# Optimization experiments

Hardware: AMD Instinct MI355X
Metric: run time of the kernel (lower is better)

## Reference

```python
import jax, jax.numpy as jnp
import numpy as np

T = 2048          # tokens
HID = 4096        # hidden_size
H = 32            # n_heads
D = 192           # head_dim
DR = 64           # qk_rope_head_dim
Q_LORA = 1536
O_LORA = 512
G = 4             # o_groups
EPS = 1e-6
MAX_POS = 4096
ROPE_BASE = 10000.0
SCALE = D ** -0.5


def _rmsnorm(x, weight=None, eps=EPS):
    # normalize over last dim in fp32, like the triton kernel / RMSNorm
    xf = x.astype(jnp.float32)
    rms_inv = jax.lax.rsqrt(jnp.mean(xf * xf, axis=-1, keepdims=True) + eps)
    out = xf * rms_inv
    if weight is not None:
        out = out * weight
    return out.astype(x.dtype)


def _apply_rope(x, cos, sin):
    # x: [..., DR]; interleaved complex rotation (deepseek-style freqs_cis mult)
    x2 = x.reshape(x.shape[:-1] + (DR // 2, 2))
    a, b = x2[..., 0], x2[..., 1]
    ra = a * cos - b * sin
    rb = a * sin + b * cos
    return jnp.stack([ra, rb], axis=-1).reshape(x.shape)


def setup_inputs() -> dict:
    key = jax.random.key(0)
    ks = jax.random.split(key, 12)
    s = lambda k, shape, scale: jax.random.normal(k, shape, dtype=jnp.float32) * scale
    x = s(ks[0], (T, HID), 1.0)
    positions = jnp.arange(T, dtype=jnp.int64)
    wq_a = s(ks[1], (Q_LORA, HID), HID ** -0.5)
    q_norm_w = jnp.ones((Q_LORA,), jnp.float32)
    wq_b = s(ks[2], (H * D, Q_LORA), Q_LORA ** -0.5)
    wkv = s(ks[3], (D, HID), HID ** -0.5)
    kv_norm_w = jnp.ones((D,), jnp.float32)
    attn_sink = s(ks[4], (H,), 1.0)
    wo_a = s(ks[5], (G * O_LORA, (H * D) // G), ((H * D) // G) ** -0.5)
    wo_b = s(ks[6], (HID, G * O_LORA), (G * O_LORA) ** -0.5)
    # precomputed rope tables [MAX_POS, DR//2]
    inv_freq = 1.0 / (ROPE_BASE ** (np.arange(0, DR, 2, dtype=np.float32) / DR))
    t = np.arange(MAX_POS, dtype=np.float32)
    freqs = np.outer(t, inv_freq)
    rope_cos = jnp.asarray(np.cos(freqs))
    rope_sin = jnp.asarray(np.sin(freqs))
    return dict(x=x, positions=positions, wq_a=wq_a, q_norm_w=q_norm_w, wq_b=wq_b,
                wkv=wkv, kv_norm_w=kv_norm_w, attn_sink=attn_sink, wo_a=wo_a,
                wo_b=wo_b, rope_cos=rope_cos, rope_sin=rope_sin)


def reference(x, positions, wq_a, q_norm_w, wq_b, wkv, kv_norm_w, attn_sink,
              wo_a, wo_b, rope_cos, rope_sin):
    cos = rope_cos[positions]  # [T, DR//2]
    sin = rope_sin[positions]

    # q path: wq_a -> RMSNorm(weighted) -> wq_b -> per-head unweighted RMSNorm -> RoPE
    q_lora = _rmsnorm(x @ wq_a.T, q_norm_w)                # [T, Q_LORA]
    q = (q_lora @ wq_b.T).reshape(T, H, D)                 # [T, H, D]
    q = _rmsnorm(q)                                        # per-head rms_normalize
    q_rope = _apply_rope(q[..., -DR:], cos[:, None, :], sin[:, None, :])
    q = jnp.concatenate([q[..., :-DR], q_rope], axis=-1)

    # shared single kv head: wkv -> kv_norm -> RoPE on rope dims
    kv = _rmsnorm(x @ wkv.T, kv_norm_w)                    # [T, D]
    kv_rope = _apply_rope(kv[..., -DR:], cos, sin)
    kv = jnp.concatenate([kv[..., :-DR], kv_rope], axis=-1)

    # MQA attention with attention sink and causal mask
    scores = jnp.einsum('thd,sd->ths', q, kv).astype(jnp.float32) * SCALE  # [T,H,S]
    causal = positions[:, None] >= positions[None, :]       # [T, S]
    scores = jnp.where(causal[:, None, :], scores, -jnp.inf)
    sink = jnp.broadcast_to(attn_sink[None, :, None], (T, H, 1))
    logits = jnp.concatenate([scores, sink], axis=-1)       # [T, H, S+1]
    probs = jax.nn.softmax(logits, axis=-1)[..., :-1]       # drop sink column
    out = jnp.einsum('ths,sd->thd', probs.astype(kv.dtype), kv)  # [T, H, D]

    # grouped low-rank output projection: wo_a per group, then wo_b
    out_g = out.reshape(T, G, (H * D) // G)
    wo_a_g = wo_a.reshape(G, O_LORA, (H * D) // G)
    o_low = jnp.einsum('tgi,goi->tgo', out_g, wo_a_g).reshape(T, G * O_LORA)
    y = o_low @ wo_b.T                                      # [T, HID]
    return y
```

## Files before the change

### kernel.cpp

```cpp
#include <hip/hip_runtime.h>
#include <hip/hip_bf16.h>

#define T_TOK 2048
#define HIDN  4096
#define NH    32
#define HD    192
#define QLORA 1536
#define OLORA 512
#define NG    4
#define NFUSE 1728

typedef unsigned short u16;
typedef __attribute__((ext_vector_type(8))) short short8;
typedef __attribute__((ext_vector_type(4))) short short4v;
typedef __attribute__((ext_vector_type(4))) float f32x4;

__device__ __forceinline__ float b2f(u16 u) {
  union { unsigned int u; float f; } x; x.u = ((unsigned int)u) << 16; return x.f;
}
__device__ __forceinline__ u16 f2b(float f) {
  union { float f; unsigned int u; } x; x.f = f;
  unsigned int r = x.u + 0x7fff + ((x.u >> 16) & 1);
  return (u16)(r >> 16);
}

#define GLOAD16(gp, lp) __builtin_amdgcn_global_load_lds( \
    (const __attribute__((address_space(1))) unsigned int*)(gp), \
    (__attribute__((address_space(3))) unsigned int*)(lp), 16, 0, 0)
#define SCHEDB() __builtin_amdgcn_sched_barrier(0)
#define SBAR()   __builtin_amdgcn_s_barrier()

__device__ __forceinline__ void cast_seg(const float* __restrict__ src,
                                         u16* __restrict__ dst, long n4,
                                         long idx, long stride) {
  for (long j = idx; j < n4; j += stride) {
    float4 v = *reinterpret_cast<const float4*>(src + j * 4);
    short4v o;
    o[0] = (short)f2b(v.x); o[1] = (short)f2b(v.y);
    o[2] = (short)f2b(v.z); o[3] = (short)f2b(v.w);
    *reinterpret_cast<short4v*>(dst + j * 4) = o;
  }
}

__global__ __launch_bounds__(256)
void cast6(const float* s0, u16* d0, long n0, const float* s1, u16* d1, long n1,
           const float* s2, u16* d2, long n2, const float* s3, u16* d3, long n3,
           const float* s4, u16* d4, long n4c, const float* s5, u16* d5, long n5) {
  long idx = (long)blockIdx.x * blockDim.x + threadIdx.x;
  long stride = (long)gridDim.x * blockDim.x;
  cast_seg(s0, d0, n0, idx, stride);
  cast_seg(s1, d1, n1, idx, stride);
  cast_seg(s2, d2, n2, idx, stride);
  cast_seg(s3, d3, n3, idx, stride);
  cast_seg(s4, d4, n4c, idx, stride);
  cast_seg(s5, d5, n5, idx, stride);
}

template <int OM>
__global__ __launch_bounds__(256)
void gemm_bt(const u16* __restrict__ A, const u16* __restrict__ B,
             void* __restrict__ Cout, int M, int N, int K,
             int lda, int ldb, int ldc,
             long a_goff, long b_goff, long c_goff) {
  A += (long)blockIdx.z * a_goff;
  B += (long)blockIdx.z * b_goff;
  __shared__ u16 As[2][128 * 32];
  __shared__ u16 Bs[2][128 * 32];
  const int tid = threadIdx.x;
  const int lane = tid & 63;
  const int wave = tid >> 6;
  const int lg = lane >> 4, lr = lane & 15;
  const int wm = (wave >> 1) * 64, wn = (wave & 1) * 64;

  int bx = blockIdx.x, by = blockIdx.y;
  {
    int nx = gridDim.x, nwg = nx * gridDim.y;
    if ((nwg & 7) == 0) {
      int lin = by * nx + bx;
      int swz = (lin & 7) * (nwg >> 3) + (lin >> 3);
      bx = swz % nx; by = swz / nx;
    }
  }
  const int m0 = bx * 128, n0 = by * 128;

  const int i0 = tid, i1 = tid + 256;
  const int ra0 = i0 >> 2, ka0 = (i0 & 3) * 8;
  const int ra1 = i1 >> 2, ka1 = (i1 & 3) * 8;
  const u16* pA0 = A + (long)(m0 + ra0) * lda + ka0;
  const u16* pA1 = A + (long)(m0 + ra1) * lda + ka1;
  int rb0 = n0 + ra0; if (rb0 > N - 1) rb0 = N - 1;
  int rb1 = n0 + ra1; if (rb1 > N - 1) rb1 = N - 1;
  const u16* pB0 = B + (long)rb0 * ldb + ka0;
  const u16* pB1 = B + (long)rb1 * ldb + ka1;
  const int woff = wave * 1024;

  f32x4 acc[4][4];
#pragma unroll
  for (int a = 0; a < 4; a++)
#pragma unroll
    for (int b = 0; b < 4; b++) acc[a][b] = f32x4{0.f, 0.f, 0.f, 0.f};

  GLOAD16(pA0, (char*)As + woff);
  GLOAD16(pA1, (char*)As + 4096 + woff);
  GLOAD16(pB0, (char*)Bs + woff);
  GLOAD16(pB1, (char*)Bs + 4096 + woff);

  const int nk = K >> 5;
  int buf = 0;
  for (int kk = 0; kk < nk; ++kk) {
    const int kn = (kk + 1 < nk) ? (kk + 1) * 32 : kk * 32;
    {
      char* dA = (char*)As + (buf ^ 1) * 8192 + woff;
      char* dB = (char*)Bs + (buf ^ 1) * 8192 + woff;
      GLOAD16(pA0 + kn, dA);
      GLOAD16(pA1 + kn, dA + 4096);
      GLOAD16(pB0 + kn, dB);
      GLOAD16(pB1 + kn, dB + 4096);
    }
    asm volatile("s_waitcnt vmcnt(4)" ::: "memory");
    SCHEDB(); SBAR(); SCHEDB();

    short8 af[4], bf[4];
#pragma unroll
    for (int i = 0; i < 4; i++)
      af[i] = *reinterpret_cast<const short8*>(&As[buf][(wm + i * 16 + lr) * 32 + lg * 8]);
#pragma unroll
    for (int i = 0; i < 4; i++)
      bf[i] = *reinterpret_cast<const short8*>(&Bs[buf][(wn + i * 16 + lr) * 32 + lg * 8]);
#pragma unroll
    for (int mi = 0; mi < 4; mi++)
#pragma unroll
      for (int ni = 0; ni < 4; ni++)
        acc[mi][ni] = __builtin_amdgcn_mfma_f32_16x16x32_bf16(af[mi], bf[ni], acc[mi][ni], 0, 0, 0);

    SCHEDB(); SBAR(); SCHEDB();
    buf ^= 1;
  }
  asm volatile("s_waitcnt vmcnt(0)" ::: "memory");

  const long cbase = (long)blockIdx.z * c_goff;
#pragma unroll
  for (int mi = 0; mi < 4; mi++) {
#pragma unroll
    for (int ni = 0; ni < 4; ni++) {
      int col = n0 + wn + ni * 16 + lr;
      if (col < N) {
#pragma unroll
        for (int i = 0; i < 4; i++) {
          int row = m0 + wm + mi * 16 + lg * 4 + i;
          float v = acc[mi][ni][i];
          if constexpr (OM == 0)
            reinterpret_cast<u16*>(Cout)[cbase + (long)row * ldc + col] = f2b(v);
          else
            reinterpret_cast<float*>(Cout)[cbase + (long)row * ldc + col] = v;
        }
      }
    }
  }
}

__global__ __launch_bounds__(256)
void rmsnorm_rows(u16* __restrict__ buf, const float* __restrict__ w) {
  const int row = blockIdx.x;
  u16* p = buf + (long)row * NFUSE;
  const int tid = threadIdx.x;
  float v[6];
  float ss = 0.f;
#pragma unroll
  for (int j = 0; j < 6; j++) { v[j] = b2f(p[tid + j * 256]); ss += v[j] * v[j]; }
#pragma unroll
  for (int m = 1; m < 64; m <<= 1) ss += __shfl_xor(ss, m);
  __shared__ float red[4];
  if ((tid & 63) == 0) red[tid >> 6] = ss;
  __syncthreads();
  ss = red[0] + red[1] + red[2] + red[3];
  float rinv = rsqrtf(ss * (1.0f / QLORA) + 1e-6f);
#pragma unroll
  for (int j = 0; j < 6; j++) p[tid + j * 256] = f2b(v[j] * rinv * w[tid + j * 256]);
}

__global__ __launch_bounds__(256)
void qnorm_rope(u16* __restrict__ q, const int* __restrict__ pos,
                const float* __restrict__ rc, const float* __restrict__ rs) {
  const int t = blockIdx.x, h = blockIdx.y * 4 + (threadIdx.x >> 6);
  u16* p = q + (long)t * (NH * HD) + h * HD;
  const int lane = threadIdx.x & 63;
  const float QS = 0.07216878364870323f * 1.4426950408889634f;
  float v0 = b2f(p[lane]), v1 = b2f(p[lane + 64]), v2 = b2f(p[lane + 128]);
  float ss = v0 * v0 + v1 * v1 + v2 * v2;
#pragma unroll
  for (int m = 1; m < 64; m <<= 1) ss += __shfl_xor(ss, m);
  float rinv = rsqrtf(ss * (1.0f / HD) + 1e-6f);
  v0 *= rinv; v1 *= rinv; v2 *= rinv;
  float partner = __shfl_xor(v2, 1);
  int pp = pos[t];
  int j = lane >> 1;
  float c = rc[pp * 32 + j], s = rs[pp * 32 + j];
  float r = ((lane & 1) == 0) ? (v2 * c - partner * s) : (partner * s + v2 * c);
  p[lane] = f2b(v0 * QS); p[lane + 64] = f2b(v1 * QS); p[lane + 128] = f2b(r * QS);
}

__global__ __launch_bounds__(256)
void kvnorm_rope(const u16* __restrict__ t1f, u16* __restrict__ kvb,
                 u16* __restrict__ kvT, const float* __restrict__ w,
                 const int* __restrict__ pos,
                 const float* __restrict__ rc, const float* __restrict__ rs) {
  const int t = blockIdx.x * 4 + (threadIdx.x >> 6);
  const u16* src = t1f + (long)t * NFUSE + QLORA;
  u16* p = kvb + (long)t * HD;
  const int lane = threadIdx.x & 63;
  float v0 = b2f(src[lane]), v1 = b2f(src[lane + 64]), v2 = b2f(src[lane + 128]);
  float ss = v0 * v0 + v1 * v1 + v2 * v2;
#pragma unroll
  for (int m = 1; m < 64; m <<= 1) ss += __shfl_xor(ss, m);
  float rinv = rsqrtf(ss * (1.0f / HD) + 1e-6f);
  v0 *= rinv * w[lane]; v1 *= rinv * w[lane + 64]; v2 *= rinv * w[lane + 128];
  float partner = __shfl_xor(v2, 1);
  int pp = pos[t];
  int j = lane >> 1;
  float c = rc[pp * 32 + j], s = rs[pp * 32 + j];
  float r = ((lane & 1) == 0) ? (v2 * c - partner * s) : (partner * s + v2 * c);
  u16 o0 = f2b(v0), o1 = f2b(v1), o2 = f2b(r);
  p[lane] = o0; p[lane + 64] = o1; p[lane + 128] = o2;
  kvT[(long)lane * T_TOK + t] = o0;
  kvT[(long)(lane + 64) * T_TOK + t] = o1;
  kvT[(long)(lane + 128) * T_TOK + t] = o2;
}

__global__ __launch_bounds__(512)
void attn(const u16* __restrict__ q, const u16* __restrict__ kv,
          const u16* __restrict__ kvT, const float* __restrict__ sink,
          u16* __restrict__ out) {
  __shared__ u16 Ks[2][64 * 192];
  __shared__ u16 Vs[2][192 * 64];
  __shared__ u16 P[8][16 * 68];
  const int tid = threadIdx.x;
  const int wave = tid >> 6, lane = tid & 63;
  const int lg = lane >> 4, lr = lane & 15;
  const int h = blockIdx.y * 8 + wave;
  u16* Pw = P[wave];

  int krow[3], koff[3], vrow[3], voff[3];
#pragma unroll
  for (int j = 0; j < 3; j++) {
    int s = tid + j * 512;
    int rk = s / 24, ck = s - rk * 24;
    krow[j] = rk; koff[j] = (ck ^ (rk & 7)) * 8;
    int rv = s >> 3, cv = s & 7;
    vrow[j] = rv; voff[j] = (cv ^ (rv & 7)) * 8;
  }
  const float skw = exp2f(sink[h] * 1.4426950408889634f);
  short8 onesf;
#pragma unroll
  for (int k = 0; k < 8; k++) onesf[k] = (short)0x3F80;
  int buf = 0;

  for (int pass = 0; pass < 2; ++pass) {
    const int qb = pass ? (int)blockIdx.x : (127 - (int)blockIdx.x);
    const int q0 = qb * 16;
    const int s_end = q0 + 16;
    const int nt = (s_end + 63) >> 6;

    short8 qf[6];
#pragma unroll
    for (int c = 0; c < 6; c++)
      qf[c] = *reinterpret_cast<const short8*>(
          q + (long)(q0 + lr) * (NH * HD) + h * HD + c * 32 + lg * 8);

    f32x4 acc[12], accS;
#pragma unroll
    for (int c = 0; c < 12; c++) acc[c] = f32x4{0.f, 0.f, 0.f, 0.f};
    accS = f32x4{0.f, 0.f, 0.f, 0.f};

    {
      char* dK = (char*)Ks[buf]; char* dV = (char*)Vs[buf];
#pragma unroll
      for (int j = 0; j < 3; j++)
        GLOAD16(kv + (long)krow[j] * HD + koff[j], dK + (tid + j * 512) * 16);
#pragma unroll
      for (int j = 0; j < 3; j++)
        GLOAD16(kvT + (long)vrow[j] * T_TOK + voff[j], dV + (tid + j * 512) * 16);
    }

    for (int t = 0; t < nt; ++t) {
      const int s0 = t * 64;
      const int sn = (t + 1 < nt) ? s0 + 64 : s0;
      {
        char* dK = (char*)Ks[buf ^ 1]; char* dV = (char*)Vs[buf ^ 1];
#pragma unroll
        for (int j = 0; j < 3; j++)
          GLOAD16(kv + (long)(sn + krow[j]) * HD + koff[j], dK + (tid + j * 512) * 16);
#pragma unroll
        for (int j = 0; j < 3; j++)
          GLOAD16(kvT + (long)vrow[j] * T_TOK + sn + voff[j], dV + (tid + j * 512) * 16);
      }
      asm volatile("s_waitcnt vmcnt(6)" ::: "memory");
      SCHEDB(); SBAR(); SCHEDB();

      const u16* Kb = Ks[buf];
      const u16* Vb = Vs[buf];
      f32x4 sc[4];
      __builtin_amdgcn_s_setprio(1);
#pragma unroll
      for (int sub = 0; sub < 4; sub++) {
        int c0 = s0 + sub * 16;
        f32x4 v = f32x4{0.f, 0.f, 0.f, 0.f};
        if (c0 < s_end) {
#pragma unroll
          for (int c = 0; c < 6; c++) {
            short8 kf = *reinterpret_cast<const short8*>(
                &Kb[((sub * 16 + lr) * HD + c * 32 + lg * 8) ^ ((lr & 7) << 3)]);
            v = __builtin_amdgcn_mfma_f32_16x16x32_bf16(qf[c], kf, v, 0, 0, 0);
          }
          int scol = c0 + lr;
#pragma unroll
          for (int i = 0; i < 4; i++) {
            int qrow = q0 + lg * 4 + i;
            v[i] = (scol <= qrow) ? v[i] : -__builtin_inff();
          }
        } else {
#pragma unroll
          for (int i = 0; i < 4; i++) v[i] = -__builtin_inff();
        }
        sc[sub] = v;
      }
      __builtin_amdgcn_s_setprio(0);

      float pr[4][4];
#pragma unroll
      for (int sub = 0; sub < 4; sub++)
#pragma unroll
        for (int i = 0; i < 4; i++) pr[sub][i] = exp2f(sc[sub][i]);
#pragma unroll
      for (int sub = 0; sub < 4; sub++)
#pragma unroll
        for (int i = 0; i < 4; i++)
          Pw[(lg * 4 + i) * 68 + sub * 16 + lr] = f2b(pr[sub][i]);
      short8 pf0 = *reinterpret_cast<const short8*>(&Pw[lr * 68 + lg * 8]);
      short8 pf1 = *reinterpret_cast<const short8*>(&Pw[lr * 68 + 32 + lg * 8]);

      __builtin_amdgcn_s_setprio(1);
#pragma unroll
      for (int c = 0; c < 12; c++) {
        short8 vf = *reinterpret_cast<const short8*>(
            &Vb[((c * 16 + lr) * 64 + lg * 8) ^ ((lr & 7) << 3)]);
        acc[c] = __builtin_amdgcn_mfma_f32_16x16x32_bf16(pf0, vf, acc[c], 0, 0, 0);
      }
      accS = __builtin_amdgcn_mfma_f32_16x16x32_bf16(pf0, onesf, accS, 0, 0, 0);
      if (s0 + 32 < s_end) {
#pragma unroll
        for (int c = 0; c < 12; c++) {
          short8 vf = *reinterpret_cast<const short8*>(
              &Vb[((c * 16 + lr) * 64 + 32 + lg * 8) ^ ((lr & 7) << 3)]);
          acc[c] = __builtin_amdgcn_mfma_f32_16x16x32_bf16(pf1, vf, acc[c], 0, 0, 0);
        }
        accS = __builtin_amdgcn_mfma_f32_16x16x32_bf16(pf1, onesf, accS, 0, 0, 0);
      }
      __builtin_amdgcn_s_setprio(0);

      SCHEDB(); SBAR(); SCHEDB();
      buf ^= 1;
    }

    asm volatile("s_waitcnt vmcnt(0)" ::: "memory");
    float rdenom[4];
#pragma unroll
    for (int i = 0; i < 4; i++) rdenom[i] = 1.0f / (skw + accS[i]);
#pragma unroll
    for (int c = 0; c < 12; c++)
#pragma unroll
      for (int i = 0; i < 4; i++) {
        int qrow = q0 + lg * 4 + i;
        out[(long)qrow * (NH * HD) + h * HD + c * 16 + lr] = f2b(acc[c][i] * rdenom[i]);
      }
    SBAR();
  }
}

extern "C" void kernel_launch(void* const* d_in, const int* in_sizes, int n_in,
                              void* d_out, int out_size, void* d_ws, size_t ws_size,
                              hipStream_t stream) {
  const float* x    = (const float*)d_in[0];
  const int* pos    = (const int*)d_in[1];
  const float* wq_a = (const float*)d_in[2];
  const float* q_nw = (const float*)d_in[3];
  const float* wq_b = (const float*)d_in[4];
  const float* wkv  = (const float*)d_in[5];
  const float* kvnw = (const float*)d_in[6];
  const float* sink = (const float*)d_in[7];
  const float* wo_a = (const float*)d_in[8];
  const float* wo_b = (const float*)d_in[9];
  const float* rcos = (const float*)d_in[10];
  const float* rsin = (const float*)d_in[11];
  float* y = (float*)d_out;

  char* ws = (char*)d_ws;
  size_t off = 0;
  auto alloc = [&](size_t bytes) -> void* {
    void* p = ws + off;
    off += (bytes + 255) & ~(size_t)255;
    return p;
  };
  u16* xb   = (u16*)alloc((size_t)T_TOK * HIDN * 2);
  u16* wqab = (u16*)alloc((size_t)QLORA * HIDN * 2);
  u16* wkvb = (u16*)alloc((size_t)HD * HIDN * 2);
  u16* wqbb = (u16*)alloc((size_t)NH * HD * QLORA * 2);
  u16* woab = (u16*)alloc((size_t)NG * OLORA * 1536 * 2);
  u16* wobb = (u16*)alloc((size_t)HIDN * NG * OLORA * 2);
  u16* t1f  = (u16*)alloc((size_t)T_TOK * NFUSE * 2);
  u16* qn   = (u16*)alloc((size_t)T_TOK * NH * HD * 2);
  u16* kvb  = (u16*)alloc((size_t)T_TOK * HD * 2);
  u16* kvT  = (u16*)alloc((size_t)HD * T_TOK * 2);
  u16* ao   = (u16*)alloc((size_t)T_TOK * NH * HD * 2);
  u16* olow = (u16*)alloc((size_t)T_TOK * NG * OLORA * 2);

  hipLaunchKernelGGL(cast6, dim3(1024), dim3(256), 0, stream,
                     x,    xb,   (long)T_TOK * HIDN / 4,
                     wq_a, wqab, (long)QLORA * HIDN / 4,
                     wkv,  wkvb, (long)HD * HIDN / 4,
                     wq_b, wqbb, (long)NH * HD * QLORA / 4,
                     wo_a, woab, (long)NG * OLORA * 1536 / 4,
                     wo_b, wobb, (long)HIDN * NG * OLORA / 4);

  hipLaunchKernelGGL((gemm_bt<0>), dim3(16, 14, 1), dim3(256), 0, stream,
                     xb, wqab, (void*)t1f, 2048, NFUSE, 4096, 4096, 4096, NFUSE, 0L, 0L, 0L);
  hipLaunchKernelGGL(rmsnorm_rows, dim3(2048), dim3(256), 0, stream, t1f, q_nw);
  hipLaunchKernelGGL(kvnorm_rope, dim3(512), dim3(256), 0, stream,
                     t1f, kvb, kvT, kvnw, pos, rcos, rsin);
  hipLaunchKernelGGL((gemm_bt<0>), dim3(16, 48, 1), dim3(256), 0, stream,
                     t1f, wqbb, (void*)qn, 2048, 6144, 1536, NFUSE, 1536, 6144, 0L, 0L, 0L);
  hipLaunchKernelGGL(qnorm_rope, dim3(2048, 8), dim3(256), 0, stream, qn, pos, rcos, rsin);
  hipLaunchKernelGGL(attn, dim3(64, 4), dim3(512), 0, stream, qn, kvb, kvT, sink, ao);
  hipLaunchKernelGGL((gemm_bt<0>), dim3(16, 4, 4), dim3(256), 0, stream,
                     ao, woab, (void*)olow, 2048, 512, 1536, 6144, 1536, 2048,
                     1536L, (long)512 * 1536, 512L);
  hipLaunchKernelGGL((gemm_bt<1>), dim3(16, 32, 1), dim3(256), 0, stream,
                     olow, wobb, (void*)y, 2048, 4096, 2048, 2048, 2048, 4096, 0L, 0L, 0L);
}
```

Measured before the change: 372.6 us.

## Process 32 query rows per wave in attention with 4-head blocks

The attention kernel now gives each wave two 16-row query tiles (32 rows) that share the same K and V fragments, and each block covers 4 heads instead of 8. Blocks shrink to 256 threads on a 32x8 grid, and each block issues twice as many async loads per KV tile. The aim is to double MFMA work per LDS read of K/V and fuse exp and masking directly into the P writes. The cost is higher register pressure from two accumulator sets, fewer waves per block, and K/V tiles being loaded by twice as many blocks.

New measurement: 413.0 us. +10.8%, slower.

```diff
diff --git a/kernel.cpp b/kernel.cpp
--- a/kernel.cpp
+++ b/kernel.cpp
@@ -227,23 +227,23 @@
   kvT[(long)(lane + 128) * T_TOK + t] = o2;
 }
 
-__global__ __launch_bounds__(512)
+__global__ __launch_bounds__(256, 1)
 void attn(const u16* __restrict__ q, const u16* __restrict__ kv,
           const u16* __restrict__ kvT, const float* __restrict__ sink,
           u16* __restrict__ out) {
   __shared__ u16 Ks[2][64 * 192];
   __shared__ u16 Vs[2][192 * 64];
-  __shared__ u16 P[8][16 * 68];
+  __shared__ u16 P[4][32 * 68];
   const int tid = threadIdx.x;
   const int wave = tid >> 6, lane = tid & 63;
   const int lg = lane >> 4, lr = lane & 15;
-  const int h = blockIdx.y * 8 + wave;
+  const int h = blockIdx.y * 4 + wave;
   u16* Pw = P[wave];
 
-  int krow[3], koff[3], vrow[3], voff[3];
-#pragma unroll
-  for (int j = 0; j < 3; j++) {
-    int s = tid + j * 512;
+  int krow[6], koff[6], vrow[6], voff[6];
+#pragma unroll
+  for (int j = 0; j < 6; j++) {
+    int s = tid + j * 256;
     int rk = s / 24, ck = s - rk * 24;
     krow[j] = rk; koff[j] = (ck ^ (rk & 7)) * 8;
     int rv = s >> 3, cv = s & 7;
@@ -256,30 +256,34 @@
   int buf = 0;
 
   for (int pass = 0; pass < 2; ++pass) {
-    const int qb = pass ? (int)blockIdx.x : (127 - (int)blockIdx.x);
-    const int q0 = qb * 16;
-    const int s_end = q0 + 16;
+    const int qb = pass ? (int)blockIdx.x : (63 - (int)blockIdx.x);
+    const int q0 = qb * 32;
+    const int s_end = q0 + 32;
     const int nt = (s_end + 63) >> 6;
 
-    short8 qf[6];
-#pragma unroll
-    for (int c = 0; c < 6; c++)
-      qf[c] = *reinterpret_cast<const short8*>(
+    short8 qf0[6], qf1[6];
+#pragma unroll
+    for (int c = 0; c < 6; c++) {
+      qf0[c] = *reinterpret_cast<const short8*>(
           q + (long)(q0 + lr) * (NH * HD) + h * HD + c * 32 + lg * 8);
-
-    f32x4 acc[12], accS;
-#pragma unroll
-    for (int c = 0; c < 12; c++) acc[c] = f32x4{0.f, 0.f, 0.f, 0.f};
-    accS = f32x4{0.f, 0.f, 0.f, 0.f};
+      qf1[c] = *reinterpret_cast<const short8*>(
+          q + (long)(q0 + 16 + lr) * (NH * HD) + h * HD + c * 32 + lg * 8);
+    }
+
+    f32x4 acc0[12], acc1[12], accS0, accS1;
+#pragma unroll
+    for (int c = 0; c < 12; c++) { acc0[c] = f32x4{0.f,0.f,0.f,0.f}; acc1[c] = f32x4{0.f,0.f,0.f,0.f}; }
+    accS0 = f32x4{0.f, 0.f, 0.f, 0.f};
+    accS1 = f32x4{0.f, 0.f, 0.f, 0.f};
 
     {
       char* dK = (char*)Ks[buf]; char* dV = (char*)Vs[buf];
 #pragma unroll
-      for (int j = 0; j < 3; j++)
-        GLOAD16(kv + (long)krow[j] * HD + koff[j], dK + (tid + j * 512) * 16);
-#pragma unroll
-      for (int j = 0; j < 3; j++)
-        GLOAD16(kvT + (long)vrow[j] * T_TOK + voff[j], dV + (tid + j * 512) * 16);
+      for (int j = 0; j < 6; j++)
+        GLOAD16(kv + (long)krow[j] * HD + koff[j], dK + (tid + j * 256) * 16);
+#pragma unroll
+      for (int j = 0; j < 6; j++)
+        GLOAD16(kvT + (long)vrow[j] * T_TOK + voff[j], dV + (tid + j * 256) * 16);
     }
 
     for (int t = 0; t < nt; ++t) {
@@ -288,73 +292,76 @@
       {
         char* dK = (char*)Ks[buf ^ 1]; char* dV = (char*)Vs[buf ^ 1];
 #pragma unroll
-        for (int j = 0; j < 3; j++)
-          GLOAD16(kv + (long)(sn + krow[j]) * HD + koff[j], dK + (tid + j * 512) * 16);
-#pragma unroll
-        for (int j = 0; j < 3; j++)
-          GLOAD16(kvT + (long)vrow[j] * T_TOK + sn + voff[j], dV + (tid + j * 512) * 16);
-      }
-      asm volatile("s_waitcnt vmcnt(6)" ::: "memory");
+        for (int j = 0; j < 6; j++)
+          GLOAD16(kv + (long)(sn + krow[j]) * HD + koff[j], dK + (tid + j * 256) * 16);
+#pragma unroll
+        for (int j = 0; j < 6; j++)
+          GLOAD16(kvT + (long)vrow[j] * T_TOK + sn + voff[j], dV + (tid + j * 256) * 16);
+      }
+      asm volatile("s_waitcnt vmcnt(12)" ::: "memory");
       SCHEDB(); SBAR(); SCHEDB();
 
       const u16* Kb = Ks[buf];
       const u16* Vb = Vs[buf];
-      f32x4 sc[4];
-      __builtin_amdgcn_s_setprio(1);
+
 #pragma unroll
       for (int sub = 0; sub < 4; sub++) {
         int c0 = s0 + sub * 16;
-        f32x4 v = f32x4{0.f, 0.f, 0.f, 0.f};
         if (c0 < s_end) {
+          f32x4 v0 = f32x4{0.f, 0.f, 0.f, 0.f};
+          f32x4 v1 = f32x4{0.f, 0.f, 0.f, 0.f};
+          __builtin_amdgcn_s_setprio(1);
 #pragma unroll
           for (int c = 0; c < 6; c++) {
             short8 kf = *reinterpret_cast<const short8*>(
                 &Kb[((sub * 16 + lr) * HD + c * 32 + lg * 8) ^ ((lr & 7) << 3)]);
-            v = __builtin_amdgcn_mfma_f32_16x16x32_bf16(qf[c], kf, v, 0, 0, 0);
+            v0 = __builtin_amdgcn_mfma_f32_16x16x32_bf16(qf0[c], kf, v0, 0, 0, 0);
+            v1 = __builtin_amdgcn_mfma_f32_16x16x32_bf16(qf1[c], kf, v1, 0, 0, 0);
           }
+          __builtin_amdgcn_s_setprio(0);
           int scol = c0 + lr;
 #pragma unroll
           for (int i = 0; i < 4; i++) {
-            int qrow = q0 + lg * 4 + i;
-            v[i] = (scol <= qrow) ? v[i] : -__builtin_inff();
+            int qrow0 = q0 + lg * 4 + i;
+            float p0 = (scol <= qrow0) ? exp2f(v0[i]) : 0.f;
+            float p1 = (scol <= qrow0 + 16) ? exp2f(v1[i]) : 0.f;
+            Pw[(lg * 4 + i) * 68 + sub * 16 + lr] = f2b(p0);
+            Pw[(16 + lg * 4 + i) * 68 + sub * 16 + lr] = f2b(p1);
           }
         } else {
 #pragma unroll
-          for (int i = 0; i < 4; i++) v[i] = -__builtin_inff();
+          for (int i = 0; i < 4; i++) {
+            Pw[(lg * 4 + i) * 68 + sub * 16 + lr] = 0;
+            Pw[(16 + lg * 4 + i) * 68 + sub * 16 + lr] = 0;
+          }
         }
-        sc[sub] = v;
-      }
-      __builtin_amdgcn_s_setprio(0);
-
-      float pr[4][4];
-#pragma unroll
-      for (int sub = 0; sub < 4; sub++)
-#pragma unroll
-        for (int i = 0; i < 4; i++) pr[sub][i] = exp2f(sc[sub][i]);
-#pragma unroll
-      for (int sub = 0; sub < 4; sub++)
-#pragma unroll
-        for (int i = 0; i < 4; i++)
-          Pw[(lg * 4 + i) * 68 + sub * 16 + lr] = f2b(pr[sub][i]);
-      short8 pf0 = *reinterpret_cast<const short8*>(&Pw[lr * 68 + lg * 8]);
-      short8 pf1 = *reinterpret_cast<const short8*>(&Pw[lr * 68 + 32 + lg * 8]);
+      }
+
+      short8 pf00 = *reinterpret_cast<const short8*>(&Pw[lr * 68 + lg * 8]);
+      short8 pf01 = *reinterpret_cast<const short8*>(&Pw[lr * 68 + 32 + lg * 8]);
+      short8 pf10 = *reinterpret_cast<const short8*>(&Pw[(16 + lr) * 68 + lg * 8]);
+      short8 pf11 = *reinterpret_cast<const short8*>(&Pw[(16 + lr) * 68 + 32 + lg * 8]);
 
       __builtin_amdgcn_s_setprio(1);
 #pragma unroll
       for (int c = 0; c < 12; c++) {
         short8 vf = *reinterpret_cast<const short8*>(
             &Vb[((c * 16 + lr) * 64 + lg * 8) ^ ((lr & 7) << 3)]);
-        acc[c] = __builtin_amdgcn_mfma_f32_16x16x32_bf16(pf0, vf, acc[c], 0, 0, 0);
-      }
-      accS = __builtin_amdgcn_mfma_f32_16x16x32_bf16(pf0, onesf, accS, 0, 0, 0);
+        acc0[c] = __builtin_amdgcn_mfma_f32_16x16x32_bf16(pf00, vf, acc0[c], 0, 0, 0);
+        acc1[c] = __builtin_amdgcn_mfma_f32_16x16x32_bf16(pf10, vf, acc1[c], 0, 0, 0);
+      }
+      accS0 = __builtin_amdgcn_mfma_f32_16x16x32_bf16(pf00, onesf, accS0, 0, 0, 0);
+      accS1 = __builtin_amdgcn_mfma_f32_16x16x32_bf16(pf10, onesf, accS1, 0, 0, 0);
       if (s0 + 32 < s_end) {
 #pragma unroll
         for (int c = 0; c < 12; c++) {
           short8 vf = *reinterpret_cast<const short8*>(
               &Vb[((c * 16 + lr) * 64 + 32 + lg * 8) ^ ((lr & 7) << 3)]);
-          acc[c] = __builtin_amdgcn_mfma_f32_16x16x32_bf16(pf1, vf, acc[c], 0, 0, 0);
+          acc0[c] = __builtin_amdgcn_mfma_f32_16x16x32_bf16(pf01, vf, acc0[c], 0, 0, 0);
+          acc1[c] = __builtin_amdgcn_mfma_f32_16x16x32_bf16(pf11, vf, acc1[c], 0, 0, 0);
         }
-        accS = __builtin_amdgcn_mfma_f32_16x16x32_bf16(pf1, onesf, accS, 0, 0, 0);
+        accS0 = __builtin_amdgcn_mfma_f32_16x16x32_bf16(pf01, onesf, accS0, 0, 0, 0);
+        accS1 = __builtin_amdgcn_mfma_f32_16x16x32_bf16(pf11, onesf, accS1, 0, 0, 0);
       }
       __builtin_amdgcn_s_setprio(0);
 
@@ -363,15 +370,19 @@
     }
 
     asm volatile("s_waitcnt vmcnt(0)" ::: "memory");
-    float rdenom[4];
-#pragma unroll
-    for (int i = 0; i < 4; i++) rdenom[i] = 1.0f / (skw + accS[i]);
+    float rd0[4], rd1[4];
+#pragma unroll
+    for (int i = 0; i < 4; i++) {
+      rd0[i] = 1.0f / (skw + accS0[i]);
+      rd1[i] = 1.0f / (skw + accS1[i]);
+    }
 #pragma unroll
     for (int c = 0; c < 12; c++)
 #pragma unroll
       for (int i = 0; i < 4; i++) {
-        int qrow = q0 + lg * 4 + i;
-        out[(long)qrow * (NH * HD) + h * HD + c * 16 + lr] = f2b(acc[c][i] * rdenom[i]);
+        int qrow0 = q0 + lg * 4 + i;
+        out[(long)qrow0 * (NH * HD) + h * HD + c * 16 + lr] = f2b(acc0[c][i] * rd0[i]);
+        out[(long)(qrow0 + 16) * (NH * HD) + h * HD + c * 16 + lr] = f2b(acc1[c][i] * rd1[i]);
       }
     SBAR();
   }
@@ -430,7 +441,7 @@
   hipLaunchKernelGGL((gemm_bt<0>), dim3(16, 48, 1), dim3(256), 0, stream,
                      t1f, wqbb, (void*)qn, 2048, 6144, 1536, NFUSE, 1536, 6144, 0L, 0L, 0L);
   hipLaunchKernelGGL(qnorm_rope, dim3(2048, 8), dim3(256), 0, stream, qn, pos, rcos, rsin);
-  hipLaunchKernelGGL(attn, dim3(64, 4), dim3(512), 0, stream, qn, kvb, kvT, sink, ao);
+  hipLaunchKernelGGL(attn, dim3(32, 8), dim3(256), 0, stream, qn, kvb, kvT, sink, ao);
   hipLaunchKernelGGL((gemm_bt<0>), dim3(16, 4, 4), dim3(256), 0, stream,
                      ao, woab, (void*)olow, 2048, 512, 1536, 6144, 1536, 2048,
                      1536L, (long)512 * 1536, 512L);
```

## Switch attention to 32x32x16 MFMA tiles with single-pass 32-row query blocks

Applied to the files above, without the earlier changes.

The attention kernel now uses 32x32x16 bf16 MFMAs and gives each block one 32-row query tile. Previously each block ran two 16-row passes with 16x16x32 MFMAs. The goal is more work per MFMA and fewer K/V tile reloads, because each tile loaded into shared memory now serves 32 query rows at once. Masking is folded into the exp step, and launch bounds ask for two blocks per CU. The trade-off is that the old pairing of long and short query blocks for load balance is gone, and register pressure rises from the f32x16 accumulators.

Result: slower. 437.3 us (+17.4%).

```diff
diff --git a/kernel.cpp b/kernel.cpp
--- a/kernel.cpp
+++ b/kernel.cpp
@@ -14,6 +14,7 @@
 typedef __attribute__((ext_vector_type(8))) short short8;
 typedef __attribute__((ext_vector_type(4))) short short4v;
 typedef __attribute__((ext_vector_type(4))) float f32x4;
+typedef __attribute__((ext_vector_type(16))) float f32x16;
 
 __device__ __forceinline__ float b2f(u16 u) {
   union { unsigned int u; float f; } x; x.u = ((unsigned int)u) << 16; return x.f;
@@ -227,16 +228,16 @@
   kvT[(long)(lane + 128) * T_TOK + t] = o2;
 }
 
-__global__ __launch_bounds__(512)
+__global__ __launch_bounds__(512, 2)
 void attn(const u16* __restrict__ q, const u16* __restrict__ kv,
           const u16* __restrict__ kvT, const float* __restrict__ sink,
           u16* __restrict__ out) {
   __shared__ u16 Ks[2][64 * 192];
   __shared__ u16 Vs[2][192 * 64];
-  __shared__ u16 P[8][16 * 68];
+  __shared__ u16 P[8][32 * 68];
   const int tid = threadIdx.x;
   const int wave = tid >> 6, lane = tid & 63;
-  const int lg = lane >> 4, lr = lane & 15;
+  const int l5 = lane >> 5, l31 = lane & 31;
   const int h = blockIdx.y * 8 + wave;
   u16* Pw = P[wave];
 
@@ -253,127 +254,124 @@
   short8 onesf;
 #pragma unroll
   for (int k = 0; k < 8; k++) onesf[k] = (short)0x3F80;
+
+  const int qb = 63 - (int)blockIdx.x;
+  const int q0 = qb * 32;
+  const int s_end = q0 + 32;
+  const int nt = (s_end + 63) >> 6;
+
+  short8 qf[12];
+#pragma unroll
+  for (int kk = 0; kk < 12; ++kk)
+    qf[kk] = *reinterpret_cast<const short8*>(
+        q + (long)(q0 + l31) * (NH * HD) + h * HD + kk * 16 + l5 * 8);
+
+  f32x16 acc0, acc1, acc2, acc3, acc4, acc5, accS;
+  acc0 = acc1 = acc2 = acc3 = acc4 = acc5 = accS = (f32x16)(0.f);
+
+  {
+    char* dK = (char*)Ks[0]; char* dV = (char*)Vs[0];
+#pragma unroll
+    for (int j = 0; j < 3; j++)
+      GLOAD16(kv + (long)krow[j] * HD + koff[j], dK + (tid + j * 512) * 16);
+#pragma unroll
+    for (int j = 0; j < 3; j++)
+      GLOAD16(kvT + (long)vrow[j] * T_TOK + voff[j], dV + (tid + j * 512) * 16);
+  }
+
   int buf = 0;
-
-  for (int pass = 0; pass < 2; ++pass) {
-    const int qb = pass ? (int)blockIdx.x : (127 - (int)blockIdx.x);
-    const int q0 = qb * 16;
-    const int s_end = q0 + 16;
-    const int nt = (s_end + 63) >> 6;
-
-    short8 qf[6];
-#pragma unroll
-    for (int c = 0; c < 6; c++)
-      qf[c] = *reinterpret_cast<const short8*>(
-          q + (long)(q0 + lr) * (NH * HD) + h * HD + c * 32 + lg * 8);
-
-    f32x4 acc[12], accS;
-#pragma unroll
-    for (int c = 0; c < 12; c++) acc[c] = f32x4{0.f, 0.f, 0.f, 0.f};
-    accS = f32x4{0.f, 0.f, 0.f, 0.f};
-
+  for (int t = 0; t < nt; ++t) {
+    const int s0 = t * 64;
+    const int sn = (t + 1 < nt) ? s0 + 64 : s0;
     {
-      char* dK = (char*)Ks[buf]; char* dV = (char*)Vs[buf];
+      char* dK = (char*)Ks[buf ^ 1]; char* dV = (char*)Vs[buf ^ 1];
 #pragma unroll
       for (int j = 0; j < 3; j++)
-        GLOAD16(kv + (long)krow[j] * HD + koff[j], dK + (tid + j * 512) * 16);
+        GLOAD16(kv + (long)(sn + krow[j]) * HD + koff[j], dK + (tid + j * 512) * 16);
 #pragma unroll
       for (int j = 0; j < 3; j++)
-        GLOAD16(kvT + (long)vrow[j] * T_TOK + voff[j], dV + (tid + j * 512) * 16);
-    }
-
-    for (int t = 0; t < nt; ++t) {
-      const int s0 = t * 64;
-      const int sn = (t + 1 < nt) ? s0 + 64 : s0;
-      {
-        char* dK = (char*)Ks[buf ^ 1]; char* dV = (char*)Vs[buf ^ 1];
-#pragma unroll
-        for (int j = 0; j < 3; j++)
-          GLOAD16(kv + (long)(sn + krow[j]) * HD + koff[j], dK + (tid + j * 512) * 16);
-#pragma unroll
-        for (int j = 0; j < 3; j++)
-          GLOAD16(kvT + (long)vrow[j] * T_TOK + sn + voff[j], dV + (tid + j * 512) * 16);
+        GLOAD16(kvT + (long)vrow[j] * T_TOK + sn + voff[j], dV + (tid + j * 512) * 16);
+    }
+    asm volatile("s_waitcnt vmcnt(6)" ::: "memory");
+    SCHEDB(); SBAR(); SCHEDB();
+
+    const u16* Kb = Ks[buf];
+    const u16* Vb = Vs[buf];
+
+#pragma unroll
+    for (int st = 0; st < 2; ++st) {
+      const int c0 = s0 + st * 32;
+      const int prow0 = st * 32 + l31;
+      if (c0 < s_end) {
+        f32x16 v = (f32x16)(0.f);
+        __builtin_amdgcn_s_setprio(1);
+#pragma unroll
+        for (int kk = 0; kk < 12; ++kk) {
+          short8 kf = *reinterpret_cast<const short8*>(
+              &Kb[((st * 32 + l31) * HD + kk * 16 + l5 * 8) ^ ((l31 & 7) << 3)]);
+          v = __builtin_amdgcn_mfma_f32_32x32x16_bf16(qf[kk], kf, v, 0, 0, 0);
+        }
+        __builtin_amdgcn_s_setprio(0);
+        const int scol = c0 + l31;
+#pragma unroll
+        for (int r = 0; r < 16; ++r) {
+          int row = (r & 3) + 8 * (r >> 2) + 4 * l5;
+          float p = (scol <= q0 + row) ? exp2f(v[r]) : 0.f;
+          Pw[row * 68 + prow0] = f2b(p);
+        }
+      } else {
+#pragma unroll
+        for (int r = 0; r < 16; ++r) {
+          int row = (r & 3) + 8 * (r >> 2) + 4 * l5;
+          Pw[row * 68 + prow0] = 0;
+        }
       }
-      asm volatile("s_waitcnt vmcnt(6)" ::: "memory");
-      SCHEDB(); SBAR(); SCHEDB();
-
-      const u16* Kb = Ks[buf];
-      const u16* Vb = Vs[buf];
-      f32x4 sc[4];
-      __builtin_amdgcn_s_setprio(1);
-#pragma unroll
-      for (int sub = 0; sub < 4; sub++) {
-        int c0 = s0 + sub * 16;
-        f32x4 v = f32x4{0.f, 0.f, 0.f, 0.f};
-        if (c0 < s_end) {
-#pragma unroll
-          for (int c = 0; c < 6; c++) {
-            short8 kf = *reinterpret_cast<const short8*>(
-                &Kb[((sub * 16 + lr) * HD + c * 32 + lg * 8) ^ ((lr & 7) << 3)]);
-            v = __builtin_amdgcn_mfma_f32_16x16x32_bf16(qf[c], kf, v, 0, 0, 0);
-          }
-          int scol = c0 + lr;
-#pragma unroll
-          for (int i = 0; i < 4; i++) {
-            int qrow = q0 + lg * 4 + i;
-            v[i] = (scol <= qrow) ? v[i] : -__builtin_inff();
-          }
-        } else {
-#pragma unroll
-          for (int i = 0; i < 4; i++) v[i] = -__builtin_inff();
-        }
-        sc[sub] = v;
-      }
-      __builtin_amdgcn_s_setprio(0);
-
-      float pr[4][4];
-#pragma unroll
-      for (int sub = 0; sub < 4; sub++)
-#pragma unroll
-        for (int i = 0; i < 4; i++) pr[sub][i] = exp2f(sc[sub][i]);
-#pragma unroll
-      for (int sub = 0; sub < 4; sub++)
-#pragma unroll
-        for (int i = 0; i < 4; i++)
-          Pw[(lg * 4 + i) * 68 + sub * 16 + lr] = f2b(pr[sub][i]);
-      short8 pf0 = *reinterpret_cast<const short8*>(&Pw[lr * 68 + lg * 8]);
-      short8 pf1 = *reinterpret_cast<const short8*>(&Pw[lr * 68 + 32 + lg * 8]);
-
-      __builtin_amdgcn_s_setprio(1);
-#pragma unroll
-      for (int c = 0; c < 12; c++) {
-        short8 vf = *reinterpret_cast<const short8*>(
-            &Vb[((c * 16 + lr) * 64 + lg * 8) ^ ((lr & 7) << 3)]);
-        acc[c] = __builtin_amdgcn_mfma_f32_16x16x32_bf16(pf0, vf, acc[c], 0, 0, 0);
-      }
-      accS = __builtin_amdgcn_mfma_f32_16x16x32_bf16(pf0, onesf, accS, 0, 0, 0);
-      if (s0 + 32 < s_end) {
-#pragma unroll
-        for (int c = 0; c < 12; c++) {
-          short8 vf = *reinterpret_cast<const short8*>(
-              &Vb[((c * 16 + lr) * 64 + 32 + lg * 8) ^ ((lr & 7) << 3)]);
-          acc[c] = __builtin_amdgcn_mfma_f32_16x16x32_bf16(pf1, vf, acc[c], 0, 0, 0);
-        }
-        accS = __builtin_amdgcn_mfma_f32_16x16x32_bf16(pf1, onesf, accS, 0, 0, 0);
-      }
-      __builtin_amdgcn_s_setprio(0);
-
-      SCHEDB(); SBAR(); SCHEDB();
-      buf ^= 1;
-    }
-
-    asm volatile("s_waitcnt vmcnt(0)" ::: "memory");
-    float rdenom[4];
-#pragma unroll
-    for (int i = 0; i < 4; i++) rdenom[i] = 1.0f / (skw + accS[i]);
-#pragma unroll
-    for (int c = 0; c < 12; c++)
-#pragma unroll
-      for (int i = 0; i < 4; i++) {
-        int qrow = q0 + lg * 4 + i;
-        out[(long)qrow * (NH * HD) + h * HD + c * 16 + lr] = f2b(acc[c][i] * rdenom[i]);
-      }
-    SBAR();
+    }
+
+    __builtin_amdgcn_s_setprio(1);
+#pragma unroll
+    for (int kk = 0; kk < 4; ++kk) {
+      short8 pa = *reinterpret_cast<const short8*>(&Pw[l31 * 68 + kk * 16 + l5 * 8]);
+      short8 vf0 = *reinterpret_cast<const short8*>(
+          &Vb[((0 * 32 + l31) * 64 + kk * 16 + l5 * 8) ^ ((l31 & 7) << 3)]);
+      short8 vf1 = *reinterpret_cast<const short8*>(
+          &Vb[((1 * 32 + l31) * 64 + kk * 16 + l5 * 8) ^ ((l31 & 7) << 3)]);
+      short8 vf2 = *reinterpret_cast<const short8*>(
+          &Vb[((2 * 32 + l31) * 64 + kk * 16 + l5 * 8) ^ ((l31 & 7) << 3)]);
+      short8 vf3 = *reinterpret_cast<const short8*>(
+          &Vb[((3 * 32 + l31) * 64 + kk * 16 + l5 * 8) ^ ((l31 & 7) << 3)]);
+      short8 vf4 = *reinterpret_cast<const short8*>(
+          &Vb[((4 * 32 + l31) * 64 + kk * 16 + l5 * 8) ^ ((l31 & 7) << 3)]);
+      short8 vf5 = *reinterpret_cast<const short8*>(
+          &Vb[((5 * 32 + l31) * 64 + kk * 16 + l5 * 8) ^ ((l31 & 7) << 3)]);
+      acc0 = __builtin_amdgcn_mfma_f32_32x32x16_bf16(pa, vf0, acc0, 0, 0, 0);
+      acc1 = __builtin_amdgcn_mfma_f32_32x32x16_bf16(pa, vf1, acc1, 0, 0, 0);
+      acc2 = __builtin_amdgcn_mfma_f32_32x32x16_bf16(pa, vf2, acc2, 0, 0, 0);
+      acc3 = __builtin_amdgcn_mfma_f32_32x32x16_bf16(pa, vf3, acc3, 0, 0, 0);
+      acc4 = __builtin_amdgcn_mfma_f32_32x32x16_bf16(pa, vf4, acc4, 0, 0, 0);
+      acc5 = __builtin_amdgcn_mfma_f32_32x32x16_bf16(pa, vf5, acc5, 0, 0, 0);
+      accS = __builtin_amdgcn_mfma_f32_32x32x16_bf16(pa, onesf, accS, 0, 0, 0);
+    }
+    __builtin_amdgcn_s_setprio(0);
+
+    SCHEDB(); SBAR(); SCHEDB();
+    buf ^= 1;
+  }
+  asm volatile("s_waitcnt vmcnt(0)" ::: "memory");
+
+  float rd[16];
+#pragma unroll
+  for (int r = 0; r < 16; ++r) rd[r] = 1.0f / (skw + accS[r]);
+#pragma unroll
+  for (int r = 0; r < 16; ++r) {
+    int qrow = q0 + (r & 3) + 8 * (r >> 2) + 4 * l5;
+    u16* op = out + (long)qrow * (NH * HD) + h * HD + l31;
+    op[0]   = f2b(acc0[r] * rd[r]);
+    op[32]  = f2b(acc1[r] * rd[r]);
+    op[64]  = f2b(acc2[r] * rd[r]);
+    op[96]  = f2b(acc3[r] * rd[r]);
+    op[128] = f2b(acc4[r] * rd[r]);
+    op[160] = f2b(acc5[r] * rd[r]);
   }
 }
 
```

## Fuse kv norm into q rmsnorm kernel and read V directly from global

Applied to the files above, without the earlier changes.

Merges the kv RMSNorm+RoPE kernel into the q-lora rmsnorm kernel, with one wave per row doing the kv part, which saves a launch. In attention, the LDS double-buffered staging of V (kvT) is removed and V fragments are read straight from global/L2 inside the PV MFMA loop. This halves LDS usage and async loads but puts global-load latency directly on the MFMA critical path, which could stall it.

New measurement: 509.7 us. 1.37x slower.

```diff
diff --git a/kernel.cpp b/kernel.cpp
--- a/kernel.cpp
+++ b/kernel.cpp
@@ -160,7 +160,10 @@
 }
 
 __global__ __launch_bounds__(256)
-void rmsnorm_rows(u16* __restrict__ buf, const float* __restrict__ w) {
+void rmsnorm_kv(u16* __restrict__ buf, const float* __restrict__ w,
+                u16* __restrict__ kvb, u16* __restrict__ kvT,
+                const float* __restrict__ kvnw, const int* __restrict__ pos,
+                const float* __restrict__ rc, const float* __restrict__ rs) {
   const int row = blockIdx.x;
   u16* p = buf + (long)row * NFUSE;
   const int tid = threadIdx.x;
@@ -177,6 +180,28 @@
   float rinv = rsqrtf(ss * (1.0f / QLORA) + 1e-6f);
 #pragma unroll
   for (int j = 0; j < 6; j++) p[tid + j * 256] = f2b(v[j] * rinv * w[tid + j * 256]);
+
+  if (tid < 64) {
+    const u16* src = p + QLORA;
+    const int lane = tid;
+    float v0 = b2f(src[lane]), v1 = b2f(src[lane + 64]), v2 = b2f(src[lane + 128]);
+    float s2 = v0 * v0 + v1 * v1 + v2 * v2;
+#pragma unroll
+    for (int m = 1; m < 64; m <<= 1) s2 += __shfl_xor(s2, m);
+    float ri = rsqrtf(s2 * (1.0f / HD) + 1e-6f);
+    v0 *= ri * kvnw[lane]; v1 *= ri * kvnw[lane + 64]; v2 *= ri * kvnw[lane + 128];
+    float partner = __shfl_xor(v2, 1);
+    int pp = pos[row];
+    int j = lane >> 1;
+    float c = rc[pp * 32 + j], s = rs[pp * 32 + j];
+    float r = ((lane & 1) == 0) ? (v2 * c - partner * s) : (partner * s + v2 * c);
+    u16 o0 = f2b(v0), o1 = f2b(v1), o2 = f2b(r);
+    u16* kp = kvb + (long)row * HD;
+    kp[lane] = o0; kp[lane + 64] = o1; kp[lane + 128] = o2;
+    kvT[(long)lane * T_TOK + row] = o0;
+    kvT[(long)(lane + 64) * T_TOK + row] = o1;
+    kvT[(long)(lane + 128) * T_TOK + row] = o2;
+  }
 }
 
 __global__ __launch_bounds__(256)
@@ -200,39 +225,11 @@
   p[lane] = f2b(v0 * QS); p[lane + 64] = f2b(v1 * QS); p[lane + 128] = f2b(r * QS);
 }
 
-__global__ __launch_bounds__(256)
-void kvnorm_rope(const u16* __restrict__ t1f, u16* __restrict__ kvb,
-                 u16* __restrict__ kvT, const float* __restrict__ w,
-                 const int* __restrict__ pos,
-                 const float* __restrict__ rc, const float* __restrict__ rs) {
-  const int t = blockIdx.x * 4 + (threadIdx.x >> 6);
-  const u16* src = t1f + (long)t * NFUSE + QLORA;
-  u16* p = kvb + (long)t * HD;
-  const int lane = threadIdx.x & 63;
-  float v0 = b2f(src[lane]), v1 = b2f(src[lane + 64]), v2 = b2f(src[lane + 128]);
-  float ss = v0 * v0 + v1 * v1 + v2 * v2;
-#pragma unroll
-  for (int m = 1; m < 64; m <<= 1) ss += __shfl_xor(ss, m);
-  float rinv = rsqrtf(ss * (1.0f / HD) + 1e-6f);
-  v0 *= rinv * w[lane]; v1 *= rinv * w[lane + 64]; v2 *= rinv * w[lane + 128];
-  float partner = __shfl_xor(v2, 1);
-  int pp = pos[t];
-  int j = lane >> 1;
-  float c = rc[pp * 32 + j], s = rs[pp * 32 + j];
-  float r = ((lane & 1) == 0) ? (v2 * c - partner * s) : (partner * s + v2 * c);
-  u16 o0 = f2b(v0), o1 = f2b(v1), o2 = f2b(r);
-  p[lane] = o0; p[lane + 64] = o1; p[lane + 128] = o2;
-  kvT[(long)lane * T_TOK + t] = o0;
-  kvT[(long)(lane + 64) * T_TOK + t] = o1;
-  kvT[(long)(lane + 128) * T_TOK + t] = o2;
-}
-
 __global__ __launch_bounds__(512)
 void attn(const u16* __restrict__ q, const u16* __restrict__ kv,
           const u16* __restrict__ kvT, const float* __restrict__ sink,
           u16* __restrict__ out) {
   __shared__ u16 Ks[2][64 * 192];
-  __shared__ u16 Vs[2][192 * 64];
   __shared__ u16 P[8][16 * 68];
   const int tid = threadIdx.x;
   const int wave = tid >> 6, lane = tid & 63;
@@ -240,14 +237,12 @@
   const int h = blockIdx.y * 8 + wave;
   u16* Pw = P[wave];
 
-  int krow[3], koff[3], vrow[3], voff[3];
+  int krow[3], koff[3];
 #pragma unroll
   for (int j = 0; j < 3; j++) {
     int s = tid + j * 512;
     int rk = s / 24, ck = s - rk * 24;
     krow[j] = rk; koff[j] = (ck ^ (rk & 7)) * 8;
-    int rv = s >> 3, cv = s & 7;
-    vrow[j] = rv; voff[j] = (cv ^ (rv & 7)) * 8;
   }
   const float skw = exp2f(sink[h] * 1.4426950408889634f);
   short8 onesf;
@@ -273,32 +268,25 @@
     accS = f32x4{0.f, 0.f, 0.f, 0.f};
 
     {
-      char* dK = (char*)Ks[buf]; char* dV = (char*)Vs[buf];
+      char* dK = (char*)Ks[buf];
 #pragma unroll
       for (int j = 0; j < 3; j++)
         GLOAD16(kv + (long)krow[j] * HD + koff[j], dK + (tid + j * 512) * 16);
-#pragma unroll
-      for (int j = 0; j < 3; j++)
-        GLOAD16(kvT + (long)vrow[j] * T_TOK + voff[j], dV + (tid + j * 512) * 16);
     }
 
     for (int t = 0; t < nt; ++t) {
       const int s0 = t * 64;
       const int sn = (t + 1 < nt) ? s0 + 64 : s0;
       {
-        char* dK = (char*)Ks[buf ^ 1]; char* dV = (char*)Vs[buf ^ 1];
+        char* dK = (char*)Ks[buf ^ 1];
 #pragma unroll
         for (int j = 0; j < 3; j++)
           GLOAD16(kv + (long)(sn + krow[j]) * HD + koff[j], dK + (tid + j * 512) * 16);
-#pragma unroll
-        for (int j = 0; j < 3; j++)
-          GLOAD16(kvT + (long)vrow[j] * T_TOK + sn + voff[j], dV + (tid + j * 512) * 16);
-      }
-      asm volatile("s_waitcnt vmcnt(6)" ::: "memory");
+      }
+      asm volatile("s_waitcnt vmcnt(3)" ::: "memory");
       SCHEDB(); SBAR(); SCHEDB();
 
       const u16* Kb = Ks[buf];
-      const u16* Vb = Vs[buf];
       f32x4 sc[4];
       __builtin_amdgcn_s_setprio(1);
 #pragma unroll
@@ -343,7 +331,7 @@
 #pragma unroll
       for (int c = 0; c < 12; c++) {
         short8 vf = *reinterpret_cast<const short8*>(
-            &Vb[((c * 16 + lr) * 64 + lg * 8) ^ ((lr & 7) << 3)]);
+            kvT + (long)(c * 16 + lr) * T_TOK + s0 + lg * 8);
         acc[c] = __builtin_amdgcn_mfma_f32_16x16x32_bf16(pf0, vf, acc[c], 0, 0, 0);
       }
       accS = __builtin_amdgcn_mfma_f32_16x16x32_bf16(pf0, onesf, accS, 0, 0, 0);
@@ -351,7 +339,7 @@
 #pragma unroll
         for (int c = 0; c < 12; c++) {
           short8 vf = *reinterpret_cast<const short8*>(
-              &Vb[((c * 16 + lr) * 64 + 32 + lg * 8) ^ ((lr & 7) << 3)]);
+              kvT + (long)(c * 16 + lr) * T_TOK + s0 + 32 + lg * 8);
           acc[c] = __builtin_amdgcn_mfma_f32_16x16x32_bf16(pf1, vf, acc[c], 0, 0, 0);
         }
         accS = __builtin_amdgcn_mfma_f32_16x16x32_bf16(pf1, onesf, accS, 0, 0, 0);
@@ -424,9 +412,8 @@
 
   hipLaunchKernelGGL((gemm_bt<0>), dim3(16, 14, 1), dim3(256), 0, stream,
                      xb, wqab, (void*)t1f, 2048, NFUSE, 4096, 4096, 4096, NFUSE, 0L, 0L, 0L);
-  hipLaunchKernelGGL(rmsnorm_rows, dim3(2048), dim3(256), 0, stream, t1f, q_nw);
-  hipLaunchKernelGGL(kvnorm_rope, dim3(512), dim3(256), 0, stream,
-                     t1f, kvb, kvT, kvnw, pos, rcos, rsin);
+  hipLaunchKernelGGL(rmsnorm_kv, dim3(2048), dim3(256), 0, stream,
+                     t1f, q_nw, kvb, kvT, kvnw, pos, rcos, rsin);
   hipLaunchKernelGGL((gemm_bt<0>), dim3(16, 48, 1), dim3(256), 0, stream,
                      t1f, wqbb, (void*)qn, 2048, 6144, 1536, NFUSE, 1536, 6144, 0L, 0L, 0L);
   hipLaunchKernelGGL(qnorm_rope, dim3(2048, 8), dim3(256), 0, stream, qn, pos, rcos, rsin);
```
